# Performance work log

Hardware: AMD Instinct MI355X
Metric: run time of the kernel (lower is better)

Reference implementation:

```python
import jax, jax.numpy as jnp
import numpy as np
from jax.ops import segment_sum, segment_max

N_NODES, SEQ, D, V = 2048, 64, 256, 32000
NH, DH = 8, 32      # transformer heads, head dim
GH = 4              # GAT heads (concat=False -> mean over heads)
E = 32768
NEG_INF = -1e9


def _pe(max_len, d):
    pos = np.arange(max_len)[:, None].astype(np.float32)
    div = np.exp(np.arange(0, d, 2).astype(np.float32) * (-np.log(10000.0) / d))
    pe = np.zeros((max_len, d), np.float32)
    pe[:, 0::2] = np.sin(pos * div)
    pe[:, 1::2] = np.cos(pos * div)
    return jnp.asarray(pe)


def _ln(x, g, b, eps=1e-5):
    m = x.mean(-1, keepdims=True)
    v = jnp.var(x, axis=-1, keepdims=True)
    return (x - m) / jnp.sqrt(v + eps) * g + b


def _encoder(x, Wqkv, bqkv, Wo, bo, ln1g, ln1b, ln2g, ln2b, W1, b1, W2, b2):
    # nn.TransformerEncoder, post-norm, relu, dropout off (eval)
    for l in range(2):
        qkv = x @ Wqkv[l] + bqkv[l]
        q, k, v = jnp.split(qkv, 3, -1)
        hds = lambda t: t.reshape(N_NODES, SEQ, NH, DH).transpose(0, 2, 1, 3)
        q, k, v = hds(q), hds(k), hds(v)
        att = jax.nn.softmax(jnp.einsum('bhqd,bhkd->bhqk', q, k) / np.sqrt(DH).astype(np.float32), -1)
        o = jnp.einsum('bhqk,bhkd->bhqd', att, v).transpose(0, 2, 1, 3).reshape(N_NODES, SEQ, D)
        x = _ln(x + o @ Wo[l] + bo[l], ln1g[l], ln1b[l])
        ff = jax.nn.relu(x @ W1[l] + b1[l]) @ W2[l] + b2[l]
        x = _ln(x + ff, ln2g[l], ln2b[l])
    return x


def _gat(xt, W, b, asrc, adst, src, dst, emask):
    # PyG GATConv(heads=4, concat=False): self-loops added, LeakyReLU(0.2),
    # softmax over incoming edges per destination, mean over heads, + bias.
    x = (xt @ W).reshape(N_NODES, GH, D)              # [N,GH,D]
    a_s = jnp.sum(x * asrc, -1)                        # [N,GH]
    a_d = jnp.sum(x * adst, -1)
    e = jax.nn.leaky_relu(a_s[src] + a_d[dst], 0.2)    # [E,GH]
    e = jnp.where(emask[:, None], e, NEG_INF)
    e_self = jax.nn.leaky_relu(a_s + a_d, 0.2)         # [N,GH] self loops
    m = jnp.maximum(segment_max(e, dst, num_segments=N_NODES), e_self)
    w = jnp.where(emask[:, None], jnp.exp(e - m[dst]), 0.0)
    w_self = jnp.exp(e_self - m)
    denom = segment_sum(w, dst, num_segments=N_NODES) + w_self
    num = segment_sum(w[:, :, None] * x[src], dst, num_segments=N_NODES) + w_self[:, :, None] * x
    return (num / denom[:, :, None]).mean(1) + b


def setup_inputs():
    key = jax.random.key(0)
    ks = iter(jax.random.split(key, 40))
    g = lambda shape, s=0.02: jax.random.normal(next(ks), shape, jnp.float32) * s
    return dict(
        tok_emb=g((V, D)),
        enc_Wqkv=g((2, D, 3 * D)), enc_bqkv=jnp.zeros((2, 3 * D)),
        enc_Wo=g((2, D, D)), enc_bo=jnp.zeros((2, D)),
        enc_ln1_g=jnp.ones((2, D)), enc_ln1_b=jnp.zeros((2, D)),
        enc_ln2_g=jnp.ones((2, D)), enc_ln2_b=jnp.zeros((2, D)),
        enc_W1=g((2, D, D)), enc_b1=jnp.zeros((2, D)),
        enc_W2=g((2, D, D)), enc_b2=jnp.zeros((2, D)),
        type_emb=g((10, D)),
        msg_W=g((3, D, D)), msg_b=jnp.zeros((3, D)),
        gat_W=g((4, D, GH * D)), gat_b=jnp.zeros((4, D)),
        gat_asrc=g((4, GH, D)), gat_adst=g((4, GH, D)),
        sp_W1=g((D, 512)), sp_b1=jnp.zeros((512,)),
        sp_W2=g((512, D)), sp_b2=jnp.zeros((D,)),
        log_c=jnp.zeros((1,)),
        rule_token_seqs=jax.random.randint(next(ks), (N_NODES, SEQ), 0, V),
        rule_types=jax.random.randint(next(ks), (N_NODES,), 0, 10),
        edge_index=jax.random.randint(next(ks), (2, E), 0, N_NODES),
        edge_type=jax.random.randint(next(ks), (E,), 0, 3),
    )


def reference(tok_emb, enc_Wqkv, enc_bqkv, enc_Wo, enc_bo, enc_ln1_g, enc_ln1_b,
              enc_ln2_g, enc_ln2_b, enc_W1, enc_b1, enc_W2, enc_b2, type_emb,
              msg_W, msg_b, gat_W, gat_b, gat_asrc, gat_adst,
              sp_W1, sp_b1, sp_W2, sp_b2, log_c,
              rule_token_seqs, rule_types, edge_index, edge_type):
    # logic encoder
    x = tok_emb[rule_token_seqs] * np.sqrt(D).astype(np.float32) + _pe(SEQ, D)[None]
    x = _encoder(x, enc_Wqkv, enc_bqkv, enc_Wo, enc_bo, enc_ln1_g, enc_ln1_b,
                 enc_ln2_g, enc_ln2_b, enc_W1, enc_b1, enc_W2, enc_b2)
    h = x.mean(1) + type_emb[rule_types]                 # node_features [N,D]
    # logical GNN: per-relation linear + GATConv, summed, residual, relu
    src, dst = edge_index[0], edge_index[1]
    for l in range(4):
        h_new = 0.0
        for r in range(3):
            th = h @ msg_W[r] + msg_b[r]
            h_new = h_new + _gat(th, gat_W[l], gat_b[l], gat_asrc[l], gat_adst[l],
                                 src, dst, edge_type == r)
        h = jax.nn.relu(h + h_new)
    pos = jax.nn.relu(h @ sp_W1 + sp_b1) @ sp_W2 + sp_b2
    tang = jnp.tanh(pos) * 2.0
    st = tang * jnp.sqrt(jnp.exp(log_c))                 # scaled tangent [N,D]
    # Lorentz exp_map0 of v = [0, st]: ||v||_L = ||st||
    r = jnp.maximum(jnp.linalg.norm(st, axis=-1, keepdims=True), 1e-8)
    return jnp.concatenate([jnp.cosh(r), jnp.sinh(r) / r * st], -1)  # [N, D+1]
```

## Files before the change

kernel.cpp:

```cpp
#include <hip/hip_runtime.h>
#include <hip/hip_bf16.h>

#define NN 2048
#define SEQL 64
#define DIM 256
#define NHEAD 8
#define EDGES 32768
#define CHUNKS 2
#define CN (NN / CHUNKS)
#define CROWS (CN * SEQL)

typedef __attribute__((ext_vector_type(8))) short short8;
typedef __attribute__((ext_vector_type(4))) float f32x4;
typedef __attribute__((ext_vector_type(4))) unsigned short us4;
typedef unsigned short ushort_t;

__device__ __forceinline__ float us2f(unsigned short u) {
    union { unsigned int i; float f; } x; x.i = ((unsigned int)u) << 16; return x.f;
}
__device__ __forceinline__ unsigned short f2us(float f) {
    union { float f; unsigned int i; } u; u.f = f;
    unsigned int r = u.i + 0x7fffu + ((u.i >> 16) & 1u);
    return (unsigned short)(r >> 16);
}
__device__ __forceinline__ float lrelu02(float v) { return v < 0.f ? 0.2f * v : v; }

__device__ __forceinline__ void gload_lds16(const void* g, void* l) {
    __builtin_amdgcn_global_load_lds(
        (const __attribute__((address_space(1))) unsigned int*)g,
        (__attribute__((address_space(3))) unsigned int*)l, 16, 0, 0);
}

__global__ void sniff_kernel(const unsigned int* __restrict__ w, int* __restrict__ flag) {
    __shared__ int cnt;
    if (threadIdx.x == 0) cnt = 0;
    __syncthreads();
    unsigned int v = w[(size_t)threadIdx.x * 509];
    unsigned int e_lo = (v >> 7) & 0xffu;
    if (e_lo >= 0x6eu && e_lo <= 0x7fu) atomicAdd(&cnt, 1);
    __syncthreads();
    if (threadIdx.x == 0) *flag = (cnt > 128) ? 1 : 0;
}

#define NE 33
struct ConvArgs {
    const void* src[NE];
    unsigned int soff[NE];
    unsigned int off[NE + 1];
    unsigned int nel[NE];
    unsigned short ncol[NE];
    unsigned char klog2[NE];
};

__global__ void convert_kernel(ConvArgs a, const int* __restrict__ flag,
                               ushort_t* __restrict__ dst, unsigned int total) {
    const int bf = *flag;
    for (unsigned int i = blockIdx.x * 256 + threadIdx.x; i < total; i += gridDim.x * 256) {
        int e = 0;
        while (a.off[e + 1] <= i) ++e;
        unsigned int j = i - a.off[e];
        ushort_t v = 0;
        if (j < a.nel[e]) {
            unsigned int sidx;
            if (a.klog2[e]) {
                unsigned int K = 1u << a.klog2[e];
                unsigned int k = j & (K - 1), n = j >> a.klog2[e];
                sidx = k * (unsigned int)a.ncol[e] + n;
            } else sidx = j;
            sidx += a.soff[e];
            if (bf) v = ((const ushort_t*)a.src[e])[sidx];
            else    v = f2us(((const float*)a.src[e])[sidx]);
        }
        dst[i] = v;
    }
}

template <bool RELU, bool OUT_BF16>
__global__ __launch_bounds__(256) void gemm_bt(
    const ushort_t* __restrict__ A, const ushort_t* __restrict__ BT,
    const ushort_t* __restrict__ bias, void* __restrict__ C,
    int M, int N, int K, int lda, size_t a_off_z, size_t c_off_z)
{
    __shared__ __align__(16) short a_lds[128][32];
    __shared__ __align__(16) short b_lds[128][32];

    const int tid  = threadIdx.x;
    const int lane = tid & 63;
    const int wave = tid >> 6;
    const int wr = wave >> 1, wc = wave & 1;
    const size_t mbase = (size_t)blockIdx.x * 128;
    const size_t nbase = (size_t)blockIdx.y * 128;
    A += (size_t)blockIdx.z * a_off_z;
    const size_t czoff = (size_t)blockIdx.z * c_off_z;

    f32x4 acc[4][4];
    const f32x4 fzero = {0.f, 0.f, 0.f, 0.f};
#pragma unroll
    for (int i = 0; i < 4; ++i)
#pragma unroll
        for (int j = 0; j < 4; ++j) acc[i][j] = fzero;

    const int srow = tid >> 2;
    const int skc  = (tid & 3) * 8;
    short* lbA = &a_lds[0][0] + wave * 512;
    short* lbB = &b_lds[0][0] + wave * 512;
    const int rl = lane & 15;
    const int kf = (lane >> 4) * 8;

    for (int k0 = 0; k0 < K; k0 += 32) {
        __syncthreads();
        gload_lds16(A  + (mbase + srow)      * (size_t)lda + k0 + skc, lbA);
        gload_lds16(A  + (mbase + srow + 64) * (size_t)lda + k0 + skc, lbA + 2048);
        gload_lds16(BT + (nbase + srow)      * (size_t)K   + k0 + skc, lbB);
        gload_lds16(BT + (nbase + srow + 64) * (size_t)K   + k0 + skc, lbB + 2048);
        __syncthreads();

        short8 af[4], bfr[4];
#pragma unroll
        for (int m = 0; m < 4; ++m) af[m]  = *(const short8*)&a_lds[wr * 64 + m * 16 + rl][kf];
#pragma unroll
        for (int n = 0; n < 4; ++n) bfr[n] = *(const short8*)&b_lds[wc * 64 + n * 16 + rl][kf];
#pragma unroll
        for (int m = 0; m < 4; ++m)
#pragma unroll
            for (int n = 0; n < 4; ++n)
                acc[m][n] = __builtin_amdgcn_mfma_f32_16x16x32_bf16(af[m], bfr[n], acc[m][n], 0, 0, 0);
    }

    const int rq = (lane >> 4) * 4;
#pragma unroll
    for (int m = 0; m < 4; ++m) {
#pragma unroll
        for (int n = 0; n < 4; ++n) {
            size_t gcol = nbase + wc * 64 + n * 16 + rl;
            float bv = bias ? us2f(bias[gcol]) : 0.f;
#pragma unroll
            for (int q = 0; q < 4; ++q) {
                size_t grow = mbase + wr * 64 + m * 16 + rq + q;
                float v = acc[m][n][q] + bv;
                if (RELU) v = fmaxf(v, 0.f);
                if (OUT_BF16) ((ushort_t*)C)[czoff + grow * N + gcol] = f2us(v);
                else          ((float*)C)[czoff + grow * N + gcol] = v;
            }
        }
    }
}

__global__ __launch_bounds__(512) void gemm_ln(
    const ushort_t* __restrict__ A, const ushort_t* __restrict__ BT,
    const ushort_t* __restrict__ bias, ushort_t* __restrict__ X,
    const ushort_t* __restrict__ gg, const ushort_t* __restrict__ bb, int K)
{
    __shared__ __align__(16) short a_lds[128][32];
    __shared__ __align__(16) short b_lds[256][32];
    __shared__ float st_part[128][8];
    __shared__ float st_fin[128][2];

    const int tid  = threadIdx.x;
    const int lane = tid & 63;
    const int wave = tid >> 6;
    const int wr = wave >> 2, wc = wave & 3;
    const size_t mbase = (size_t)blockIdx.x * 128;

    f32x4 acc[4][4];
    const f32x4 fzero = {0.f, 0.f, 0.f, 0.f};
#pragma unroll
    for (int i = 0; i < 4; ++i)
#pragma unroll
        for (int j = 0; j < 4; ++j) acc[i][j] = fzero;

    const int srow = tid >> 2;
    const int skc  = (tid & 3) * 8;
    short* lbA = &a_lds[0][0] + wave * 512;
    short* lbB = &b_lds[0][0] + wave * 512;
    const int rl = lane & 15;
    const int g  = lane >> 4;
    const int kf = g * 8;

    for (int k0 = 0; k0 < K; k0 += 32) {
        __syncthreads();
        gload_lds16(A  + (mbase + srow) * (size_t)K + k0 + skc, lbA);
        gload_lds16(BT + (size_t)srow         * K + k0 + skc, lbB);
        gload_lds16(BT + (size_t)(srow + 128) * K + k0 + skc, lbB + 4096);
        __syncthreads();

        short8 af[4], bfr[4];
#pragma unroll
        for (int m = 0; m < 4; ++m) af[m]  = *(const short8*)&a_lds[wr * 64 + m * 16 + rl][kf];
#pragma unroll
        for (int n = 0; n < 4; ++n) bfr[n] = *(const short8*)&b_lds[wc * 64 + n * 16 + rl][kf];
#pragma unroll
        for (int m = 0; m < 4; ++m)
#pragma unroll
            for (int n = 0; n < 4; ++n)
                acc[m][n] = __builtin_amdgcn_mfma_f32_16x16x32_bf16(af[m], bfr[n], acc[m][n], 0, 0, 0);
    }

#pragma unroll
    for (int m = 0; m < 4; ++m)
#pragma unroll
        for (int n = 0; n < 4; ++n) {
            int gcol = wc * 64 + n * 16 + rl;
            float bv = us2f(bias[gcol]);
#pragma unroll
            for (int r = 0; r < 4; ++r) {
                size_t grow = mbase + wr * 64 + m * 16 + g * 4 + r;
                acc[m][n][r] += bv + us2f(X[grow * 256 + gcol]);
            }
        }
#pragma unroll
    for (int m = 0; m < 4; ++m)
#pragma unroll
        for (int r = 0; r < 4; ++r) {
            float ps = 0.f, pq = 0.f;
#pragma unroll
            for (int n = 0; n < 4; ++n) { float v = acc[m][n][r]; ps += v; pq += v * v; }
#pragma unroll
            for (int off = 1; off < 16; off <<= 1) { ps += __shfl_xor(ps, off); pq += __shfl_xor(pq, off); }
            if (rl == 0) {
                int row = wr * 64 + m * 16 + g * 4 + r;
                st_part[row][wc] = ps;
                st_part[row][4 + wc] = pq;
            }
        }
    __syncthreads();
    if (tid < 128) {
        float s = st_part[tid][0] + st_part[tid][1] + st_part[tid][2] + st_part[tid][3];
        float q = st_part[tid][4] + st_part[tid][5] + st_part[tid][6] + st_part[tid][7];
        float mean = s * (1.f / 256.f);
        float var = q * (1.f / 256.f) - mean * mean;
        st_fin[tid][0] = mean;
        st_fin[tid][1] = rsqrtf(var + 1e-5f);
    }
    __syncthreads();
#pragma unroll
    for (int m = 0; m < 4; ++m)
#pragma unroll
        for (int n = 0; n < 4; ++n) {
            int gcol = wc * 64 + n * 16 + rl;
            float gv = us2f(gg[gcol]), bv = us2f(bb[gcol]);
#pragma unroll
            for (int r = 0; r < 4; ++r) {
                int row = wr * 64 + m * 16 + g * 4 + r;
                float out = (acc[m][n][r] - st_fin[row][0]) * st_fin[row][1] * gv + bv;
                X[(mbase + row) * 256 + gcol] = f2us(out);
            }
        }
}

__global__ __launch_bounds__(128) void attn_mfma(const ushort_t* __restrict__ qkv,
                                                 ushort_t* __restrict__ O) {
    __shared__ ushort_t smem[2][6912];
    const int w = threadIdx.x >> 6, lane = threadIdx.x & 63;
    const int h = blockIdx.y * 2 + w;
    const int rl = lane & 15, g = lane >> 4;
    const size_t rowbase = (size_t)blockIdx.x * 64;
    ushort_t* vt = smem[w];
    ushort_t* pl = smem[w] + 2304;

    const ushort_t* vp = qkv + (rowbase + lane) * 768 + 512 + h * 32;
#pragma unroll
    for (int i = 0; i < 4; ++i) {
        union { short8 v; ushort_t s[8]; } u;
        u.v = *(const short8*)(vp + i * 8);
#pragma unroll
        for (int j = 0; j < 8; ++j) vt[(i * 8 + j) * 72 + lane] = u.s[j];
    }

    short8 kf[4], qf[4];
#pragma unroll
    for (int t = 0; t < 4; ++t) {
        kf[t] = *(const short8*)(qkv + (rowbase + t * 16 + rl) * 768 + 256 + h * 32 + g * 8);
        qf[t] = *(const short8*)(qkv + (rowbase + t * 16 + rl) * 768 +       h * 32 + g * 8);
    }

    f32x4 s[4][4];
    const f32x4 fzero = {0.f, 0.f, 0.f, 0.f};
#pragma unroll
    for (int kt = 0; kt < 4; ++kt)
#pragma unroll
        for (int qt = 0; qt < 4; ++qt) s[kt][qt] = fzero;
#pragma unroll
    for (int kt = 0; kt < 4; ++kt)
#pragma unroll
        for (int qt = 0; qt < 4; ++qt)
            s[kt][qt] = __builtin_amdgcn_mfma_f32_16x16x32_bf16(kf[kt], qf[qt], s[kt][qt], 0, 0, 0);

    const float sc = 0.17677669529663687f;
    float inv[4];
#pragma unroll
    for (int qt = 0; qt < 4; ++qt) {
        float m = -1e30f;
#pragma unroll
        for (int kt = 0; kt < 4; ++kt)
#pragma unroll
            for (int r = 0; r < 4; ++r) { s[kt][qt][r] *= sc; m = fmaxf(m, s[kt][qt][r]); }
        m = fmaxf(m, __shfl_xor(m, 16));
        m = fmaxf(m, __shfl_xor(m, 32));
        float sum = 0.f;
#pragma unroll
        for (int kt = 0; kt < 4; ++kt)
#pragma unroll
            for (int r = 0; r < 4; ++r) { float e = __expf(s[kt][qt][r] - m); s[kt][qt][r] = e; sum += e; }
        sum += __shfl_xor(sum, 16);
        sum += __shfl_xor(sum, 32);
        inv[qt] = 1.f / sum;
    }

#pragma unroll
    for (int qt = 0; qt < 4; ++qt)
#pragma unroll
        for (int kt = 0; kt < 4; ++kt) {
            us4 pk;
#pragma unroll
            for (int r = 0; r < 4; ++r) pk[r] = f2us(s[kt][qt][r] * inv[qt]);
            *(us4*)&pl[(qt * 16 + rl) * 72 + kt * 16 + g * 4] = pk;
        }
    asm volatile("s_waitcnt lgkmcnt(0)" ::: "memory");
    __builtin_amdgcn_sched_barrier(0);

    f32x4 o[2][4];
#pragma unroll
    for (int dt = 0; dt < 2; ++dt)
#pragma unroll
        for (int qt = 0; qt < 4; ++qt) o[dt][qt] = fzero;
#pragma unroll
    for (int ks = 0; ks < 2; ++ks) {
        short8 va[2];
#pragma unroll
        for (int dt = 0; dt < 2; ++dt)
            va[dt] = *(const short8*)&vt[(dt * 16 + rl) * 72 + ks * 32 + g * 8];
#pragma unroll
        for (int qt = 0; qt < 4; ++qt) {
            short8 pb = *(const short8*)&pl[(qt * 16 + rl) * 72 + ks * 32 + g * 8];
#pragma unroll
            for (int dt = 0; dt < 2; ++dt)
                o[dt][qt] = __builtin_amdgcn_mfma_f32_16x16x32_bf16(va[dt], pb, o[dt][qt], 0, 0, 0);
        }
    }

#pragma unroll
    for (int dt = 0; dt < 2; ++dt)
#pragma unroll
        for (int qt = 0; qt < 4; ++qt) {
            us4 ov;
#pragma unroll
            for (int r = 0; r < 4; ++r) ov[r] = f2us(o[dt][qt][r]);
            *(us4*)&pl[(qt * 16 + rl) * 40 + dt * 16 + g * 4] = ov;
        }
    asm volatile("s_waitcnt lgkmcnt(0)" ::: "memory");
    __builtin_amdgcn_sched_barrier(0);
    ushort_t* op = O + (rowbase + lane) * 256 + h * 32;
#pragma unroll
    for (int t = 0; t < 4; ++t)
        *(short8*)(op + t * 8) = *(const short8*)&pl[lane * 40 + t * 8];
}

__global__ void pe_kernel(float* __restrict__ pe) {
    int s = blockIdx.x, d = threadIdx.x;
    int i = d >> 1;
    float freq = __expf((float)(2 * i) * (-9.210340371976184f / 256.f));
    float ang = (float)s * freq;
    pe[s * DIM + d] = (d & 1) ? cosf(ang) : sinf(ang);
}

__global__ void embed_kernel(const void* __restrict__ tok_emb,
                             const int* __restrict__ flag,
                             const int* __restrict__ tokens,
                             const float* __restrict__ pe,
                             ushort_t* __restrict__ X, int row0) {
    int lr = blockIdx.x, d = threadIdx.x;
    int grow = row0 + lr;
    int tok = tokens[grow];
    int s = grow & 63;
    size_t idx = (size_t)tok * DIM + d;
    float tv = (*flag) ? us2f(((const ushort_t*)tok_emb)[idx])
                       : ((const float*)tok_emb)[idx];
    float v = tv * 16.f + pe[s * DIM + d];
    X[(size_t)lr * DIM + d] = f2us(v);
}

__global__ void mean_kernel(const ushort_t* __restrict__ Xc,
                            const ushort_t* __restrict__ type_emb,
                            const int* __restrict__ rtypes,
                            float* __restrict__ h, ushort_t* __restrict__ hb, int n0) {
    int nl = blockIdx.x, d = threadIdx.x;
    float acc = 0.f;
    for (int s = 0; s < 64; ++s) acc += us2f(Xc[((size_t)nl * 64 + s) * DIM + d]);
    int n = n0 + nl;
    float val = acc * (1.f / 64.f) + us2f(type_emb[(size_t)rtypes[n] * DIM + d]);
    h[(size_t)n * DIM + d] = val;
    hb[(size_t)n * DIM + d] = f2us(val);
}

__global__ void hist_kernel(const int* __restrict__ ei, int* __restrict__ counts) {
    int e = blockIdx.x * 256 + threadIdx.x;
    if (e < EDGES) atomicAdd(&counts[ei[EDGES + e]], 1);
}
__global__ __launch_bounds__(256) void scan_kernel(const int* __restrict__ counts,
                                                   int* __restrict__ indptr,
                                                   int* __restrict__ cursor) {
    __shared__ int part[256];
    int t = threadIdx.x;
    int local[8]; int s = 0;
#pragma unroll
    for (int i = 0; i < 8; ++i) { local[i] = s; s += counts[t * 8 + i]; }
    part[t] = s;
    __syncthreads();
    for (int d = 1; d < 256; d <<= 1) {
        int val = (t >= d) ? part[t - d] : 0;
        __syncthreads();
        part[t] += val;
        __syncthreads();
    }
    int base = part[t] - s;
#pragma unroll
    for (int i = 0; i < 8; ++i) { int v = base + local[i]; indptr[t * 8 + i] = v; cursor[t * 8 + i] = v; }
    if (t == 255) indptr[NN] = part[255];
}
__global__ void scatter_kernel(const int* __restrict__ ei, const int* __restrict__ et,
                               int* __restrict__ cursor, int* __restrict__ col_src,
                               int* __restrict__ col_type) {
    int e = blockIdx.x * 256 + threadIdx.x;
    if (e < EDGES) {
        int d = ei[EDGES + e];
        int pp = atomicAdd(&cursor[d], 1);
        col_src[pp] = ei[e];
        col_type[pp] = et[e];
    }
}

__global__ __launch_bounds__(256) void asad_kernel(const float* __restrict__ xg,
                                                   const ushort_t* __restrict__ asrc,
                                                   const ushort_t* __restrict__ adst,
                                                   float* __restrict__ a_s, float* __restrict__ a_d,
                                                   int l) {
    int n = blockIdx.x, r = blockIdx.y, g = threadIdx.x >> 6, lane = threadIdx.x & 63;
    const float* xp = xg + ((size_t)r * NN + n) * 1024 + g * 256 + lane * 4;
    const ushort_t* sp = asrc + ((size_t)l * 4 + g) * 256 + lane * 4;
    const ushort_t* dp = adst + ((size_t)l * 4 + g) * 256 + lane * 4;
    float ss = 0.f, dd = 0.f;
#pragma unroll
    for (int j = 0; j < 4; ++j) { float x = xp[j]; ss += x * us2f(sp[j]); dd += x * us2f(dp[j]); }
#pragma unroll
    for (int off = 32; off > 0; off >>= 1) { ss += __shfl_xor(ss, off); dd += __shfl_xor(dd, off); }
    if (lane == 0) {
        a_s[((size_t)r * NN + n) * 4 + g] = ss;
        a_d[((size_t)r * NN + n) * 4 + g] = dd;
    }
}

__global__ __launch_bounds__(256) void edge_kernel(const float* __restrict__ xg,
                                                   const float* __restrict__ a_s,
                                                   const float* __restrict__ a_d,
                                                   const int* __restrict__ indptr,
                                                   const int* __restrict__ col_src,
                                                   const int* __restrict__ col_type,
                                                   const ushort_t* __restrict__ gat_b,
                                                   float* __restrict__ hnew3, int l) {
    __shared__ float outs[4][256];
    int n = blockIdx.x, r = blockIdx.y, g = threadIdx.x >> 6, lane = threadIdx.x & 63;
    int beg = indptr[n], end = indptr[n + 1];
    const size_t rb = (size_t)r * NN;
    float adn = a_d[(rb + n) * 4 + g];
    float eself = lrelu02(a_s[(rb + n) * 4 + g] + adn);
    float m = eself;
    for (int e = beg; e < end; ++e) {
        if (col_type[e] == r) {
            float v = lrelu02(a_s[(rb + col_src[e]) * 4 + g] + adn);
            m = fmaxf(m, v);
        }
    }
    float wself = __expf(eself - m);
    float denom = wself;
    const float* xn = xg + (rb + n) * 1024 + g * 256 + lane * 4;
    float num[4];
#pragma unroll
    for (int j = 0; j < 4; ++j) num[j] = wself * xn[j];
    for (int e = beg; e < end; ++e) {
        if (col_type[e] == r) {
            int src = col_src[e];
            float v = lrelu02(a_s[(rb + src) * 4 + g] + adn);
            float w = __expf(v - m);
            denom += w;
            const float* xs = xg + (rb + src) * 1024 + g * 256 + lane * 4;
#pragma unroll
            for (int j = 0; j < 4; ++j) num[j] += w * xs[j];
        }
    }
    float invd = 1.f / denom;
#pragma unroll
    for (int j = 0; j < 4; ++j) outs[g][lane * 4 + j] = num[j] * invd;
    __syncthreads();
    int d = threadIdx.x;
    float hv = 0.25f * (outs[0][d] + outs[1][d] + outs[2][d] + outs[3][d]) + us2f(gat_b[l * 256 + d]);
    hnew3[(rb + n) * 256 + d] = hv;
}

__global__ void update_h_kernel(float* __restrict__ h, const float* __restrict__ hnew3,
                                ushort_t* __restrict__ hb) {
    size_t i = (size_t)blockIdx.x * 256 + threadIdx.x;
    float v = fmaxf(h[i] + hnew3[i] + hnew3[(size_t)NN * 256 + i] + hnew3[(size_t)2 * NN * 256 + i], 0.f);
    h[i] = v;
    hb[i] = f2us(v);
}

__global__ __launch_bounds__(64) void final_kernel(const float* __restrict__ pos,
                                                   const ushort_t* __restrict__ log_c,
                                                   const int* __restrict__ flag,
                                                   void* __restrict__ out) {
    int n = blockIdx.x, lane = threadIdx.x;
    int bf = *flag;
    float scv = sqrtf(__expf(us2f(log_c[0])));
    f32x4 pv = *(const f32x4*)&pos[(size_t)n * 256 + lane * 4];
    float st[4]; float sq = 0.f;
#pragma unroll
    for (int j = 0; j < 4; ++j) { float t = tanhf(pv[j]) * 2.f * scv; st[j] = t; sq += t * t; }
#pragma unroll
    for (int off = 32; off > 0; off >>= 1) sq += __shfl_xor(sq, off);
    float rr = fmaxf(sqrtf(sq), 1e-8f);
    float sf = sinhf(rr) / rr;
    if (bf) {
        ushort_t* o = (ushort_t*)out;
        if (lane == 0) o[(size_t)n * 257] = f2us(coshf(rr));
#pragma unroll
        for (int j = 0; j < 4; ++j) o[(size_t)n * 257 + 1 + lane * 4 + j] = f2us(sf * st[j]);
    } else {
        float* o = (float*)out;
        if (lane == 0) o[(size_t)n * 257] = coshf(rr);
#pragma unroll
        for (int j = 0; j < 4; ++j) o[(size_t)n * 257 + 1 + lane * 4 + j] = sf * st[j];
    }
}

extern "C" void kernel_launch(void* const* d_in, const int* in_sizes, int n_in,
                              void* d_out, int out_size, void* d_ws, size_t ws_size,
                              hipStream_t stream) {
    const int* tokens = (const int*)d_in[25];
    const int* rtypes = (const int*)d_in[26];
    const int* eidx   = (const int*)d_in[27];
    const int* etype  = (const int*)d_in[28];

    char* base = (char*)d_ws;
    size_t pos = 0;
    auto alloc = [&](size_t b) -> char* {
        char* r = base + pos; pos = (pos + b + 255) & ~(size_t)255; return r;
    };

    int* flag = (int*)alloc(256);

    ConvArgs ca;
    int ne = 0; unsigned int off = 0;
    auto add = [&](const void* src, unsigned int soff, unsigned int elems,
                   int klog2, int ncol) -> unsigned int {
        ca.src[ne] = src; ca.soff[ne] = soff; ca.off[ne] = off;
        ca.nel[ne] = elems; ca.klog2[ne] = (unsigned char)klog2;
        ca.ncol[ne] = (unsigned short)ncol;
        unsigned int r = off; off += (elems + 7) & ~7u; ++ne; return r;
    };
    unsigned int oWqkv = add(d_in[1], 0, 196608, 8, 768);
                         add(d_in[1], 196608, 196608, 8, 768);
    unsigned int obqkv = add(d_in[2], 0, 1536, 0, 0);
    unsigned int oWo   = add(d_in[3], 0, 65536, 8, 256);
                         add(d_in[3], 65536, 65536, 8, 256);
    unsigned int obo   = add(d_in[4], 0, 512, 0, 0);
    unsigned int oln1g = add(d_in[5], 0, 512, 0, 0);
    unsigned int oln1b = add(d_in[6], 0, 512, 0, 0);
    unsigned int oln2g = add(d_in[7], 0, 512, 0, 0);
    unsigned int oln2b = add(d_in[8], 0, 512, 0, 0);
    unsigned int oW1   = add(d_in[9], 0, 65536, 8, 256);
                         add(d_in[9], 65536, 65536, 8, 256);
    unsigned int ob1   = add(d_in[10], 0, 512, 0, 0);
    unsigned int oW2   = add(d_in[11], 0, 65536, 8, 256);
                         add(d_in[11], 65536, 65536, 8, 256);
    unsigned int ob2   = add(d_in[12], 0, 512, 0, 0);
    unsigned int otype = add(d_in[13], 0, 2560, 0, 0);
    unsigned int omsgW = add(d_in[14], 0, 65536, 8, 256);
                         add(d_in[14], 65536, 65536, 8, 256);
                         add(d_in[14], 131072, 65536, 8, 256);
    unsigned int omsgb = add(d_in[15], 0, 768, 0, 0);
    unsigned int ogatW = add(d_in[16], 0, 262144, 8, 1024);
                         add(d_in[16], 262144, 262144, 8, 1024);
                         add(d_in[16], 524288, 262144, 8, 1024);
                         add(d_in[16], 786432, 262144, 8, 1024);
    unsigned int ogatb = add(d_in[17], 0, 1024, 0, 0);
    unsigned int oasrc = add(d_in[18], 0, 4096, 0, 0);
    unsigned int oadst = add(d_in[19], 0, 4096, 0, 0);
    unsigned int ospW1 = add(d_in[20], 0, 131072, 8, 512);
    unsigned int ospb1 = add(d_in[21], 0, 512, 0, 0);
    unsigned int ospW2 = add(d_in[22], 0, 131072, 9, 256);
    unsigned int ospb2 = add(d_in[23], 0, 256, 0, 0);
    unsigned int ologc = add(d_in[24], 0, 1, 0, 0);
    ca.off[ne] = off;
    unsigned int wtotal = off;

    ushort_t* wtb   = (ushort_t*)alloc((size_t)wtotal * 2);
    float*    pe    = (float*)   alloc((size_t)SEQL * DIM * 4);
    float*    h     = (float*)   alloc((size_t)NN * DIM * 4);
    ushort_t* hb    = (ushort_t*)alloc((size_t)NN * DIM * 2);
    float*    a_s   = (float*)   alloc((size_t)3 * NN * 4 * 4);
    float*    a_d   = (float*)   alloc((size_t)3 * NN * 4 * 4);
    int*      counts = (int*)    alloc((size_t)NN * 4);
    int*      indptr = (int*)    alloc((size_t)(NN + 1) * 4);
    int*      cursor = (int*)    alloc((size_t)NN * 4);
    int*      col_src  = (int*)  alloc((size_t)EDGES * 4);
    int*      col_type = (int*)  alloc((size_t)EDGES * 4);

    size_t spos0 = pos;
    ushort_t* Xc  = (ushort_t*)alloc((size_t)CROWS * DIM * 2);
    ushort_t* QKV = (ushort_t*)alloc((size_t)CROWS * 768 * 2);
    ushort_t* Oc  = (ushort_t*)alloc((size_t)CROWS * DIM * 2);
    pos = spos0;
    ushort_t* th    = (ushort_t*)alloc((size_t)NN * 768 * 2);
    float*    xg    = (float*)   alloc((size_t)3 * NN * 1024 * 4);
    float*    hnew3 = (float*)   alloc((size_t)3 * NN * DIM * 4);
    ushort_t* thead = (ushort_t*)alloc((size_t)NN * 512 * 2);
    float*    posb  = (float*)   alloc((size_t)NN * DIM * 4);

    const ushort_t* WqkvT = wtb + oWqkv;
    const ushort_t* bqkv  = wtb + obqkv;
    const ushort_t* WoT   = wtb + oWo;
    const ushort_t* bo    = wtb + obo;
    const ushort_t* ln1g  = wtb + oln1g;
    const ushort_t* ln1b  = wtb + oln1b;
    const ushort_t* ln2g  = wtb + oln2g;
    const ushort_t* ln2b  = wtb + oln2b;
    const ushort_t* W1T   = wtb + oW1;
    const ushort_t* b1    = wtb + ob1;
    const ushort_t* W2T   = wtb + oW2;
    const ushort_t* b2    = wtb + ob2;
    const ushort_t* type_emb = wtb + otype;
    const ushort_t* msgWT = wtb + omsgW;
    const ushort_t* msg_b = wtb + omsgb;
    const ushort_t* gatWT = wtb + ogatW;
    const ushort_t* gat_b = wtb + ogatb;
    const ushort_t* gasrc = wtb + oasrc;
    const ushort_t* gadst = wtb + oadst;
    const ushort_t* spW1T = wtb + ospW1;
    const ushort_t* spb1  = wtb + ospb1;
    const ushort_t* spW2T = wtb + ospW2;
    const ushort_t* spb2  = wtb + ospb2;
    const ushort_t* log_c = wtb + ologc;

    sniff_kernel<<<1, 256, 0, stream>>>((const unsigned int*)d_in[1], flag);
    convert_kernel<<<2048, 256, 0, stream>>>(ca, flag, wtb, wtotal);

    pe_kernel<<<SEQL, DIM, 0, stream>>>(pe);
    hipMemsetAsync(counts, 0, NN * 4, stream);
    hist_kernel<<<EDGES / 256, 256, 0, stream>>>(eidx, counts);
    scan_kernel<<<1, 256, 0, stream>>>(counts, indptr, cursor);
    scatter_kernel<<<EDGES / 256, 256, 0, stream>>>(eidx, etype, cursor, col_src, col_type);

    for (int c = 0; c < CHUNKS; ++c) {
        int row0 = c * CROWS;
        embed_kernel<<<CROWS, DIM, 0, stream>>>(d_in[0], flag, tokens, pe, Xc, row0);
        for (int l = 0; l < 2; ++l) {
            gemm_bt<false, true><<<dim3(CROWS / 128, 6), 256, 0, stream>>>(
                Xc, WqkvT + (size_t)l * 196608, bqkv + l * 768, QKV, CROWS, 768, DIM, DIM, 0, 0);
            attn_mfma<<<dim3(CN, 4), 128, 0, stream>>>(QKV, Oc);
            gemm_ln<<<CROWS / 128, 512, 0, stream>>>(
                Oc, WoT + (size_t)l * 65536, bo + l * DIM, Xc, ln1g + l * DIM, ln1b + l * DIM, DIM);
            gemm_bt<true, true><<<dim3(CROWS / 128, 2), 256, 0, stream>>>(
                Xc, W1T + (size_t)l * 65536, b1 + l * DIM, Oc, CROWS, DIM, DIM, DIM, 0, 0);
            gemm_ln<<<CROWS / 128, 512, 0, stream>>>(
                Oc, W2T + (size_t)l * 65536, b2 + l * DIM, Xc, ln2g + l * DIM, ln2b + l * DIM, DIM);
        }
        mean_kernel<<<CN, DIM, 0, stream>>>(Xc, type_emb, rtypes, h, hb, c * CN);
    }

    for (int l = 0; l < 4; ++l) {
        gemm_bt<false, true><<<dim3(NN / 128, 6), 256, 0, stream>>>(
            hb, msgWT, msg_b, th, NN, 768, DIM, DIM, 0, 0);
        gemm_bt<false, false><<<dim3(NN / 128, 8, 3), 256, 0, stream>>>(
            th, gatWT + (size_t)l * 262144, nullptr, xg, NN, 1024, DIM, 768,
            (size_t)256, (size_t)NN * 1024);
        asad_kernel<<<dim3(NN, 3), 256, 0, stream>>>(xg, gasrc, gadst, a_s, a_d, l);
        edge_kernel<<<dim3(NN, 3), 256, 0, stream>>>(xg, a_s, a_d, indptr, col_src, col_type,
                                                     gat_b, hnew3, l);
        update_h_kernel<<<NN, 256, 0, stream>>>(h, hnew3, hb);
    }

    gemm_bt<true, true><<<dim3(NN / 128, 4), 256, 0, stream>>>(
        hb, spW1T, spb1, thead, NN, 512, DIM, DIM, 0, 0);
    gemm_bt<false, false><<<dim3(NN / 128, 2), 256, 0, stream>>>(
        thead, spW2T, spb2, posb, NN, DIM, 512, 512, 0, 0);
    final_kernel<<<NN, 64, 0, stream>>>(posb, log_c, flag, d_out);
}
```

Measured before the change: 1.264 ms.

## Double-buffer GEMM LDS tiles with XOR swizzle and vectorize embedding kernel

```diff
diff --git a/kernel.cpp b/kernel.cpp
--- a/kernel.cpp
+++ b/kernel.cpp
@@ -81,8 +81,8 @@
     const ushort_t* __restrict__ bias, void* __restrict__ C,
     int M, int N, int K, int lda, size_t a_off_z, size_t c_off_z)
 {
-    __shared__ __align__(16) short a_lds[128][32];
-    __shared__ __align__(16) short b_lds[128][32];
+    __shared__ __align__(16) short a_lds[2][128][32];
+    __shared__ __align__(16) short b_lds[2][128][32];
 
     const int tid  = threadIdx.x;
     const int lane = tid & 63;
@@ -101,30 +101,37 @@
         for (int j = 0; j < 4; ++j) acc[i][j] = fzero;
 
     const int srow = tid >> 2;
-    const int skc  = (tid & 3) * 8;
-    short* lbA = &a_lds[0][0] + wave * 512;
-    short* lbB = &b_lds[0][0] + wave * 512;
+    const int ksw0 = (((tid & 3) ^ ((srow >> 1) & 3)) * 8);
     const int rl = lane & 15;
-    const int kf = (lane >> 4) * 8;
-
-    for (int k0 = 0; k0 < K; k0 += 32) {
-        __syncthreads();
-        gload_lds16(A  + (mbase + srow)      * (size_t)lda + k0 + skc, lbA);
-        gload_lds16(A  + (mbase + srow + 64) * (size_t)lda + k0 + skc, lbA + 2048);
-        gload_lds16(BT + (nbase + srow)      * (size_t)K   + k0 + skc, lbB);
-        gload_lds16(BT + (nbase + srow + 64) * (size_t)K   + k0 + skc, lbB + 2048);
-        __syncthreads();
+    const int kfs = (((lane >> 4) ^ ((rl >> 1) & 3)) * 8);
+
+    const int nk = K >> 5;
+    auto stage = [&](int buf, int k0) {
+        short* lA = &a_lds[buf][0][0] + wave * 512;
+        short* lB = &b_lds[buf][0][0] + wave * 512;
+        gload_lds16(A  + (mbase + srow)      * (size_t)lda + k0 + ksw0, lA);
+        gload_lds16(A  + (mbase + srow + 64) * (size_t)lda + k0 + ksw0, lA + 2048);
+        gload_lds16(BT + (nbase + srow)      * (size_t)K   + k0 + ksw0, lB);
+        gload_lds16(BT + (nbase + srow + 64) * (size_t)K   + k0 + ksw0, lB + 2048);
+    };
+
+    stage(0, 0);
+    __syncthreads();
+    for (int t = 0; t < nk; ++t) {
+        const int cur = t & 1;
+        if (t + 1 < nk) stage(cur ^ 1, (t + 1) * 32);
 
         short8 af[4], bfr[4];
 #pragma unroll
-        for (int m = 0; m < 4; ++m) af[m]  = *(const short8*)&a_lds[wr * 64 + m * 16 + rl][kf];
-#pragma unroll
-        for (int n = 0; n < 4; ++n) bfr[n] = *(const short8*)&b_lds[wc * 64 + n * 16 + rl][kf];
+        for (int m = 0; m < 4; ++m) af[m]  = *(const short8*)&a_lds[cur][wr * 64 + m * 16 + rl][kfs];
+#pragma unroll
+        for (int n = 0; n < 4; ++n) bfr[n] = *(const short8*)&b_lds[cur][wc * 64 + n * 16 + rl][kfs];
 #pragma unroll
         for (int m = 0; m < 4; ++m)
 #pragma unroll
             for (int n = 0; n < 4; ++n)
                 acc[m][n] = __builtin_amdgcn_mfma_f32_16x16x32_bf16(af[m], bfr[n], acc[m][n], 0, 0, 0);
+        if (t + 1 < nk) __syncthreads();
     }
 
     const int rq = (lane >> 4) * 4;
@@ -151,8 +158,8 @@
     const ushort_t* __restrict__ bias, ushort_t* __restrict__ X,
     const ushort_t* __restrict__ gg, const ushort_t* __restrict__ bb, int K)
 {
-    __shared__ __align__(16) short a_lds[128][32];
-    __shared__ __align__(16) short b_lds[256][32];
+    __shared__ __align__(16) short a_lds[2][128][32];
+    __shared__ __align__(16) short b_lds[2][256][32];
     __shared__ float st_part[128][8];
     __shared__ float st_fin[128][2];
 
@@ -170,30 +177,38 @@
         for (int j = 0; j < 4; ++j) acc[i][j] = fzero;
 
     const int srow = tid >> 2;
-    const int skc  = (tid & 3) * 8;
-    short* lbA = &a_lds[0][0] + wave * 512;
-    short* lbB = &b_lds[0][0] + wave * 512;
+    const int ksw0 = (((tid & 3) ^ ((srow >> 1) & 3)) * 8);
     const int rl = lane & 15;
     const int g  = lane >> 4;
-    const int kf = g * 8;
-
-    for (int k0 = 0; k0 < K; k0 += 32) {
-        __syncthreads();
-        gload_lds16(A  + (mbase + srow) * (size_t)K + k0 + skc, lbA);
-        gload_lds16(BT + (size_t)srow         * K + k0 + skc, lbB);
-        gload_lds16(BT + (size_t)(srow + 128) * K + k0 + skc, lbB + 4096);
-        __syncthreads();
+    const int kfs = ((g ^ ((rl >> 1) & 3)) * 8);
+
+    const int nk = K >> 5;
+    auto stage = [&](int buf, int k0) {
+        gload_lds16(A  + (mbase + srow) * (size_t)K + k0 + ksw0,
+                    &a_lds[buf][0][0] + wave * 512);
+        gload_lds16(BT + (size_t)srow         * K + k0 + ksw0,
+                    &b_lds[buf][0][0] + wave * 512);
+        gload_lds16(BT + (size_t)(srow + 128) * K + k0 + ksw0,
+                    &b_lds[buf][0][0] + wave * 512 + 4096);
+    };
+
+    stage(0, 0);
+    __syncthreads();
+    for (int t = 0; t < nk; ++t) {
+        const int cur = t & 1;
+        if (t + 1 < nk) stage(cur ^ 1, (t + 1) * 32);
 
         short8 af[4], bfr[4];
 #pragma unroll
-        for (int m = 0; m < 4; ++m) af[m]  = *(const short8*)&a_lds[wr * 64 + m * 16 + rl][kf];
-#pragma unroll
-        for (int n = 0; n < 4; ++n) bfr[n] = *(const short8*)&b_lds[wc * 64 + n * 16 + rl][kf];
+        for (int m = 0; m < 4; ++m) af[m]  = *(const short8*)&a_lds[cur][wr * 64 + m * 16 + rl][kfs];
+#pragma unroll
+        for (int n = 0; n < 4; ++n) bfr[n] = *(const short8*)&b_lds[cur][wc * 64 + n * 16 + rl][kfs];
 #pragma unroll
         for (int m = 0; m < 4; ++m)
 #pragma unroll
             for (int n = 0; n < 4; ++n)
                 acc[m][n] = __builtin_amdgcn_mfma_f32_16x16x32_bf16(af[m], bfr[n], acc[m][n], 0, 0, 0);
+        if (t + 1 < nk) __syncthreads();
     }
 
 #pragma unroll
@@ -364,20 +379,29 @@
     pe[s * DIM + d] = (d & 1) ? cosf(ang) : sinf(ang);
 }
 
-__global__ void embed_kernel(const void* __restrict__ tok_emb,
-                             const int* __restrict__ flag,
-                             const int* __restrict__ tokens,
-                             const float* __restrict__ pe,
-                             ushort_t* __restrict__ X, int row0) {
-    int lr = blockIdx.x, d = threadIdx.x;
+__global__ __launch_bounds__(64) void embed_kernel(const void* __restrict__ tok_emb,
+                                                   const int* __restrict__ flag,
+                                                   const int* __restrict__ tokens,
+                                                   const float* __restrict__ pe,
+                                                   ushort_t* __restrict__ X, int row0) {
+    int lr = blockIdx.x, t = threadIdx.x;
     int grow = row0 + lr;
     int tok = tokens[grow];
     int s = grow & 63;
-    size_t idx = (size_t)tok * DIM + d;
-    float tv = (*flag) ? us2f(((const ushort_t*)tok_emb)[idx])
-                       : ((const float*)tok_emb)[idx];
-    float v = tv * 16.f + pe[s * DIM + d];
-    X[(size_t)lr * DIM + d] = f2us(v);
+    int d0 = t * 4;
+    size_t idx = (size_t)tok * DIM + d0;
+    f32x4 pv = *(const f32x4*)&pe[s * DIM + d0];
+    us4 out;
+    if (*flag) {
+        us4 tv = *(const us4*)((const ushort_t*)tok_emb + idx);
+#pragma unroll
+        for (int j = 0; j < 4; ++j) out[j] = f2us(us2f(tv[j]) * 16.f + pv[j]);
+    } else {
+        f32x4 tv = *(const f32x4*)((const float*)tok_emb + idx);
+#pragma unroll
+        for (int j = 0; j < 4; ++j) out[j] = f2us(tv[j] * 16.f + pv[j]);
+    }
+    *(us4*)&X[(size_t)lr * DIM + d0] = out;
 }
 
 __global__ void mean_kernel(const ushort_t* __restrict__ Xc,
@@ -653,7 +677,7 @@
 
     for (int c = 0; c < CHUNKS; ++c) {
         int row0 = c * CROWS;
-        embed_kernel<<<CROWS, DIM, 0, stream>>>(d_in[0], flag, tokens, pe, Xc, row0);
+        embed_kernel<<<CROWS, 64, 0, stream>>>(d_in[0], flag, tokens, pe, Xc, row0);
         for (int l = 0; l < 2; ++l) {
             gemm_bt<false, true><<<dim3(CROWS / 128, 6), 256, 0, stream>>>(
                 Xc, WqkvT + (size_t)l * 196608, bqkv + l * 768, QKV, CROWS, 768, DIM, DIM, 0, 0);
```

After: 1.192 ms. -5.7%, faster.
